# Kernel tuning notes

Measured on AMD Instinct MI355X. Metric: run time of the kernel, lower is better.

The kernel has to match this reference:

```python
import jax, jax.numpy as jnp
import numpy as np

B, N, M, DQ, DK, DV, H = 8, 1024, 1024, 512, 512, 512, 8
DS = DV // H  # dim_split = 64
NEG = -1e38


def _ln(x, g, b, eps=1e-5):
    mu = jnp.mean(x, -1, keepdims=True)
    var = jnp.mean((x - mu) ** 2, -1, keepdims=True)
    return (x - mu) * jax.lax.rsqrt(var + eps) * g + b


def setup_inputs() -> dict:
    key = jax.random.key(0)
    ks = jax.random.split(key, 16)
    s = 0.02
    return {
        "x": jax.random.normal(ks[0], (B, N, DQ), jnp.float32),
        "y": jax.random.normal(ks[1], (B, M, DK), jnp.float32),
        "x_mask": jax.random.randint(ks[2], (B, N), 0, 2).astype(bool),
        "y_mask": jax.random.randint(ks[3], (B, M), 0, 2).astype(bool),
        "Wq": jax.random.normal(ks[4], (DQ, DV), jnp.float32) * s,
        "Wk": jax.random.normal(ks[5], (DK, DV), jnp.float32) * s,
        "Wv": jax.random.normal(ks[6], (DK, DV), jnp.float32) * s,
        "Wo": jax.random.normal(ks[7], (DV, DQ), jnp.float32) * s,
        "W1": jax.random.normal(ks[8], (DQ, DQ), jnp.float32) * s,
        "b1": jnp.zeros((DQ,), jnp.float32),
        "W2": jax.random.normal(ks[9], (DQ, DQ), jnp.float32) * s,
        "b2": jnp.zeros((DQ,), jnp.float32),
        "g1": jnp.ones((DQ,), jnp.float32),
        "be1": jnp.zeros((DQ,), jnp.float32),
        "g2": jnp.ones((DQ,), jnp.float32),
        "be2": jnp.zeros((DQ,), jnp.float32),
    }


def reference(x, y, x_mask, y_mask, Wq, Wk, Wv, Wo, W1, b1, W2, b2, g1, be1, g2, be2):
    xm = x_mask[..., None]  # [B,N,1]
    ym = y_mask[..., None]  # [B,M,1]
    x = jnp.where(xm, 0.0, x)
    y = jnp.where(ym, 0.0, y)
    # projections (no bias); masked rows stay zero, re-mask as in source
    q = jnp.where(xm, 0.0, x @ Wq).reshape(B, N, H, DS)
    k = jnp.where(ym, 0.0, y @ Wk).reshape(B, M, H, DS)
    v = jnp.where(ym, 0.0, y @ Wv).reshape(B, M, H, DS)
    # scaled dot product; NOTE: scale is sqrt(dim_v), faithful to source
    sdp = jnp.einsum('bnhd,bmhd->bhnm', q, k) / np.sqrt(DV)
    mask = x_mask[:, None, :, None] | y_mask[:, None, None, :]  # [B,1,N,M]
    sdp = jnp.where(mask, NEG, sdp)
    alpha = jax.nn.softmax(sdp, axis=-1)  # softmax over keys (slot_att=False)
    att = jnp.einsum('bhnm,bmhd->bnhd', alpha, v).reshape(B, N, DV)
    att = jnp.where(xm, 0.0, att)
    o = x + att @ Wo
    o = _ln(o, g1, be1)
    ff = jax.nn.relu(o @ W1 + b1) @ W2 + b2
    o = _ln(o + ff, g2, be2)
    return jnp.where(xm, 0.0, o)
```

## Files before the change

kernel.cpp:

```cpp
#include <hip/hip_runtime.h>
#include <hip/hip_bf16.h>

typedef __bf16 bf16;
typedef __attribute__((ext_vector_type(4))) __bf16 bf16x4;
typedef __attribute__((ext_vector_type(8))) __bf16 bf16x8;
typedef __attribute__((ext_vector_type(4))) float f32x4;

#define B_ 8
#define N_ 1024
#define M_ 1024
#define H_ 8
#define ROWS_ (B_ * N_)

__device__ __forceinline__ f32x4 mfma16(bf16x8 a, bf16x8 b, f32x4 c) {
    return __builtin_amdgcn_mfma_f32_16x16x32_bf16(a, b, c, 0, 0, 0);
}

__device__ __forceinline__ void glds16(const void* g, void* l) {
    __builtin_amdgcn_global_load_lds((const __attribute__((address_space(1))) void*)g,
                                     (__attribute__((address_space(3))) void*)l, 16, 0, 0);
}

__global__ __launch_bounds__(256) void prep(const float* __restrict__ x, const float* __restrict__ y,
                                            bf16* __restrict__ Xb, bf16* __restrict__ Yb,
                                            const float* W0, const float* W1, const float* W2,
                                            const float* W3, const float* W4, const float* W5,
                                            bf16* T0, bf16* T1, bf16* T2, bf16* T3, bf16* T4, bf16* T5) {
    __shared__ float t[64][65];
    int bid = blockIdx.x;
    if (bid < 8192) {
        int i = bid * 256 + threadIdx.x;
        const float4* s;
        bf16x4* d;
        int j;
        if (i < 1048576) { s = (const float4*)x; d = (bf16x4*)Xb; j = i; }
        else             { s = (const float4*)y; d = (bf16x4*)Yb; j = i - 1048576; }
        float4 f = s[j];
        bf16x4 o = {(bf16)f.x, (bf16)f.y, (bf16)f.z, (bf16)f.w};
        d[j] = o;
        return;
    }
    int wb = bid - 8192;
    const float* srcs[6] = {W0, W1, W2, W3, W4, W5};
    bf16* dsts[6] = {T0, T1, T2, T3, T4, T5};
    const float* W = srcs[wb >> 6];
    bf16* Wt = dsts[wb >> 6];
    int tile = wb & 63;
    int k0 = (tile >> 3) * 64, n0 = (tile & 7) * 64;
    int tx = threadIdx.x & 63, ty = threadIdx.x >> 6;
#pragma unroll
    for (int j = 0; j < 16; ++j)
        t[ty + j * 4][tx] = W[(size_t)(k0 + ty + j * 4) * 512 + n0 + tx];
    __syncthreads();
#pragma unroll
    for (int j = 0; j < 16; ++j)
        Wt[(size_t)(n0 + ty + j * 4) * 512 + k0 + tx] = (bf16)t[tx][ty + j * 4];
}

__device__ __forceinline__ void gemm_core(const bf16* __restrict__ A, const bf16* __restrict__ Bt,
                                          int row0, int col0, bf16* As, bf16* Bs, f32x4 acc[2][4]) {
    int tid = threadIdx.x, wave = tid >> 6, lane = tid & 63;
    int lr = lane & 15, q4 = lane >> 4;
    const bf16* Asrc[4];
    const bf16* Bsrc[2];
#pragma unroll
    for (int s = 0; s < 4; ++s) {
        int c = tid + s * 256, r = c >> 3, bk = (c & 7) ^ (r & 7);
        Asrc[s] = A + (size_t)(row0 + r) * 512 + bk * 8;
    }
#pragma unroll
    for (int s = 0; s < 2; ++s) {
        int c = tid + s * 256, r = c >> 3, bk = (c & 7) ^ (r & 7);
        Bsrc[s] = Bt + (size_t)(col0 + r) * 512 + bk * 8;
    }
    int wb = wave * 1024;
    for (int k0 = 0; k0 < 512; k0 += 64) {
        __syncthreads();
#pragma unroll
        for (int s = 0; s < 4; ++s) glds16(Asrc[s] + k0, (char*)As + s * 4096 + wb);
#pragma unroll
        for (int s = 0; s < 2; ++s) glds16(Bsrc[s] + k0, (char*)Bs + s * 4096 + wb);
        __syncthreads();
        bf16x8 af[2][2], bfr[4][2];
#pragma unroll
        for (int rt = 0; rt < 2; ++rt) {
            int row = wave * 32 + rt * 16 + lr;
#pragma unroll
            for (int c = 0; c < 2; ++c)
                af[rt][c] = *(const bf16x8*)((const char*)As + (row * 8 + ((c * 4 + q4) ^ (row & 7))) * 16);
        }
#pragma unroll
        for (int ct = 0; ct < 4; ++ct) {
            int col = ct * 16 + lr;
#pragma unroll
            for (int c = 0; c < 2; ++c)
                bfr[ct][c] = *(const bf16x8*)((const char*)Bs + (col * 8 + ((c * 4 + q4) ^ (col & 7))) * 16);
        }
#pragma unroll
        for (int rt = 0; rt < 2; ++rt)
#pragma unroll
            for (int ct = 0; ct < 4; ++ct) {
                acc[rt][ct] = mfma16(af[rt][0], bfr[ct][0], acc[rt][ct]);
                acc[rt][ct] = mfma16(af[rt][1], bfr[ct][1], acc[rt][ct]);
            }
    }
}

__global__ __launch_bounds__(256) void proj_qkv(const bf16* __restrict__ Xb, const bf16* __restrict__ Yb,
                                                const bf16* __restrict__ Wqt, const bf16* __restrict__ Wkt,
                                                const bf16* __restrict__ Wvt,
                                                bf16* __restrict__ qb, bf16* __restrict__ kb,
                                                bf16* __restrict__ Vt) {
    __shared__ bf16 As[128 * 64];
    __shared__ bf16 Bs[64 * 64];
    int z = blockIdx.z;
    const bf16 *A, *Bt;
    int row0, col0;
    if (z == 0)      { A = Xb;  Bt = Wqt; row0 = blockIdx.x * 128; col0 = blockIdx.y * 64; }
    else if (z == 1) { A = Yb;  Bt = Wkt; row0 = blockIdx.x * 128; col0 = blockIdx.y * 64; }
    else { A = Wvt; Bt = Yb; int flat = blockIdx.y * 64 + blockIdx.x; row0 = (flat & 3) * 128; col0 = (flat >> 2) * 64; }
    const f32x4 z4 = {0.f, 0.f, 0.f, 0.f};
    f32x4 acc[2][4] = {{z4, z4, z4, z4}, {z4, z4, z4, z4}};
    gemm_core(A, Bt, row0, col0, As, Bs, acc);
    int wave = threadIdx.x >> 6, lane = threadIdx.x & 63, lr = lane & 15, q4 = lane >> 4;
    bf16* dst = (z == 0) ? qb : kb;
#pragma unroll
    for (int rt = 0; rt < 2; ++rt)
#pragma unroll
        for (int ct = 0; ct < 4; ++ct) {
            int col = col0 + ct * 16 + lr;
#pragma unroll
            for (int r = 0; r < 4; ++r) {
                int row = row0 + wave * 32 + rt * 16 + q4 * 4 + r;
                bf16 v = (bf16)acc[rt][ct][r];
                if (z < 2) dst[(size_t)row * 512 + col] = v;
                else Vt[(size_t)((col >> 10) * 512 + row) * 1024 + (col & 1023)] = v;
            }
        }
}

template <int MODE>
__global__ __launch_bounds__(256) void gemm_bt(const bf16* __restrict__ A, const bf16* __restrict__ Bt,
                                               const float* __restrict__ bias, void* __restrict__ Cout) {
    __shared__ bf16 As[128 * 64];
    __shared__ bf16 Bs[64 * 64];
    int row0 = blockIdx.x * 128, col0 = blockIdx.y * 64;
    const f32x4 z4 = {0.f, 0.f, 0.f, 0.f};
    f32x4 acc[2][4] = {{z4, z4, z4, z4}, {z4, z4, z4, z4}};
    gemm_core(A, Bt, row0, col0, As, Bs, acc);
    int wave = threadIdx.x >> 6, lane = threadIdx.x & 63, lr = lane & 15, q4 = lane >> 4;
#pragma unroll
    for (int rt = 0; rt < 2; ++rt)
#pragma unroll
        for (int ct = 0; ct < 4; ++ct) {
            int col = col0 + ct * 16 + lr;
            float bv = (MODE >= 2) ? bias[col] : 0.0f;
#pragma unroll
            for (int r = 0; r < 4; ++r) {
                int row = row0 + wave * 32 + rt * 16 + q4 * 4 + r;
                float v = acc[rt][ct][r] + bv;
                if (MODE == 3) v = fmaxf(v, 0.0f);
                if (MODE == 3) ((bf16*)Cout)[(size_t)row * 512 + col] = (bf16)v;
                else           ((float*)Cout)[(size_t)row * 512 + col] = v;
            }
        }
}

__global__ __launch_bounds__(512) void attn(const bf16* __restrict__ Q, const bf16* __restrict__ Kb,
                                            const bf16* __restrict__ Vt, const int* __restrict__ ymask,
                                            bf16* __restrict__ att) {
    __shared__ bf16 Ks[2][64 * 64];
    __shared__ bf16 Vs[2][64 * 64];
    __shared__ bf16 Ps[8][16 * 72];

    int bid = blockIdx.x;
    int bh = bid & 63, n0 = (bid >> 6) * 128;
    int b = bh >> 3, h = bh & 7;
    int tid = threadIdx.x, wave = tid >> 6, lane = tid & 63;
    int lr = lane & 15, q4 = lane >> 4;
    const float scale = 0.044194173824159216f;

    const bf16* qp = Q + (size_t)((b << 10) + n0 + wave * 16 + lr) * 512 + h * 64 + q4 * 8;
    bf16x8 aq0 = *(const bf16x8*)qp;
    bf16x8 aq1 = *(const bf16x8*)(qp + 32);

    int r = tid >> 3, bk = (tid & 7) ^ (r & 7);
    const bf16* Ksrc = Kb + (size_t)((b << 10) + r) * 512 + h * 64 + bk * 8;
    const bf16* Vsrc = Vt + (size_t)(b * 512 + h * 64 + r) * 1024 + bk * 8;
    int wb = wave * 1024;

    const f32x4 zv = {0.f, 0.f, 0.f, 0.f};
    f32x4 O[4] = {zv, zv, zv, zv};
    float lsum[4] = {0.f, 0.f, 0.f, 0.f};

    for (int m0 = 0; m0 < M_; m0 += 128) {
        int mk0 = ymask[(b << 10) + m0 + lane];
        int mk1 = ymask[(b << 10) + m0 + 64 + lane];
        __syncthreads();
        glds16(Ksrc + (size_t)m0 * 512, (char*)Ks[0] + wb);
        glds16(Ksrc + (size_t)(m0 + 64) * 512, (char*)Ks[1] + wb);
        glds16(Vsrc + m0, (char*)Vs[0] + wb);
        glds16(Vsrc + m0 + 64, (char*)Vs[1] + wb);
        __syncthreads();

#pragma unroll
        for (int half = 0; half < 2; ++half) {
            const char* K_ = (const char*)Ks[half];
            const char* V_ = (const char*)Vs[half];
            int mkh = half ? mk1 : mk0;
#pragma unroll
            for (int nt = 0; nt < 4; ++nt) {
                int krow = nt * 16 + lr;
                bf16x8 kf0 = *(const bf16x8*)(K_ + (krow * 8 + (q4 ^ (krow & 7))) * 16);
                bf16x8 kf1 = *(const bf16x8*)(K_ + (krow * 8 + ((4 + q4) ^ (krow & 7))) * 16);
                int mkv = __shfl(mkh, krow);
                f32x4 s = mfma16(aq0, kf0, zv);
                s = mfma16(aq1, kf1, s);
#pragma unroll
                for (int rr = 0; rr < 4; ++rr) {
                    float p = mkv ? 0.0f : __expf(s[rr] * scale);
                    lsum[rr] += p;
                    Ps[wave][(q4 * 4 + rr) * 72 + krow] = (bf16)p;
                }
            }
            bf16x8 ap0 = *(const bf16x8*)&Ps[wave][lr * 72 + q4 * 8];
            bf16x8 ap1 = *(const bf16x8*)&Ps[wave][lr * 72 + 32 + q4 * 8];
#pragma unroll
            for (int dt = 0; dt < 4; ++dt) {
                int vrow = dt * 16 + lr;
                bf16x8 vf0 = *(const bf16x8*)(V_ + (vrow * 8 + (q4 ^ (vrow & 7))) * 16);
                bf16x8 vf1 = *(const bf16x8*)(V_ + (vrow * 8 + ((4 + q4) ^ (vrow & 7))) * 16);
                O[dt] = mfma16(ap0, vf0, O[dt]);
                O[dt] = mfma16(ap1, vf1, O[dt]);
            }
        }
    }

#pragma unroll
    for (int rr = 0; rr < 4; ++rr) {
        float v = lsum[rr];
        v += __shfl_xor(v, 1); v += __shfl_xor(v, 2);
        v += __shfl_xor(v, 4); v += __shfl_xor(v, 8);
        lsum[rr] = (v > 0.0f) ? (1.0f / v) : 0.0f;
    }
#pragma unroll
    for (int dt = 0; dt < 4; ++dt)
#pragma unroll
        for (int rr = 0; rr < 4; ++rr) {
            int row = n0 + wave * 16 + q4 * 4 + rr;
            att[(size_t)((b << 10) + row) * 512 + h * 64 + dt * 16 + lr] =
                (bf16)(O[dt][rr] * lsum[rr]);
        }
}

__global__ __launch_bounds__(256) void ln1_k(const float* __restrict__ X, const float* __restrict__ R,
                                             const float* __restrict__ g, const float* __restrict__ be,
                                             float* __restrict__ O, bf16* __restrict__ Obf) {
    int row = blockIdx.x, t = threadIdx.x;
    size_t base = (size_t)row * 512;
    float t0 = X[base + t] + R[base + t];
    float t1 = X[base + 256 + t] + R[base + 256 + t];
    float s = t0 + t1, sq = t0 * t0 + t1 * t1;
#pragma unroll
    for (int off = 1; off < 64; off <<= 1) { s += __shfl_xor(s, off); sq += __shfl_xor(sq, off); }
    __shared__ float ls[4], lq[4];
    int w = t >> 6;
    if ((t & 63) == 0) { ls[w] = s; lq[w] = sq; }
    __syncthreads();
    s = ls[0] + ls[1] + ls[2] + ls[3];
    sq = lq[0] + lq[1] + lq[2] + lq[3];
    float mu = s * (1.0f / 512.0f);
    float var = sq * (1.0f / 512.0f) - mu * mu;
    float rs = rsqrtf(var + 1e-5f);
    float o0 = (t0 - mu) * rs * g[t] + be[t];
    float o1 = (t1 - mu) * rs * g[256 + t] + be[256 + t];
    O[base + t] = o0; O[base + 256 + t] = o1;
    Obf[base + t] = (bf16)o0; Obf[base + 256 + t] = (bf16)o1;
}

__global__ __launch_bounds__(256) void ln2_k(const float* __restrict__ O, const float* __restrict__ F,
                                             const float* __restrict__ g, const float* __restrict__ be,
                                             const int* __restrict__ xmask, float* __restrict__ out) {
    int row = blockIdx.x, t = threadIdx.x;
    size_t base = (size_t)row * 512;
    float t0 = O[base + t] + F[base + t];
    float t1 = O[base + 256 + t] + F[base + 256 + t];
    float s = t0 + t1, sq = t0 * t0 + t1 * t1;
#pragma unroll
    for (int off = 1; off < 64; off <<= 1) { s += __shfl_xor(s, off); sq += __shfl_xor(sq, off); }
    __shared__ float ls[4], lq[4];
    int w = t >> 6;
    if ((t & 63) == 0) { ls[w] = s; lq[w] = sq; }
    __syncthreads();
    s = ls[0] + ls[1] + ls[2] + ls[3];
    sq = lq[0] + lq[1] + lq[2] + lq[3];
    float mu = s * (1.0f / 512.0f);
    float var = sq * (1.0f / 512.0f) - mu * mu;
    float rs = rsqrtf(var + 1e-5f);
    int msk = xmask[row];
    float o0 = (t0 - mu) * rs * g[t] + be[t];
    float o1 = (t1 - mu) * rs * g[256 + t] + be[256 + t];
    out[base + t] = msk ? 0.0f : o0;
    out[base + 256 + t] = msk ? 0.0f : o1;
}

extern "C" void kernel_launch(void* const* d_in, const int* in_sizes, int n_in,
                              void* d_out, int out_size, void* d_ws, size_t ws_size,
                              hipStream_t stream) {
    const float* x   = (const float*)d_in[0];
    const float* y   = (const float*)d_in[1];
    const int*   xm  = (const int*)d_in[2];
    const int*   ym  = (const int*)d_in[3];
    const float* Wq  = (const float*)d_in[4];
    const float* Wk  = (const float*)d_in[5];
    const float* Wv  = (const float*)d_in[6];
    const float* Wo  = (const float*)d_in[7];
    const float* W1  = (const float*)d_in[8];
    const float* b1  = (const float*)d_in[9];
    const float* W2  = (const float*)d_in[10];
    const float* b2  = (const float*)d_in[11];
    const float* g1  = (const float*)d_in[12];
    const float* be1 = (const float*)d_in[13];
    const float* g2  = (const float*)d_in[14];
    const float* be2 = (const float*)d_in[15];

    char* ws = (char*)d_ws;
    const size_t WT_SZ  = 512 * 512 * sizeof(bf16);
    const size_t XB_SZ  = (size_t)ROWS_ * 512 * sizeof(bf16);
    const size_t F32_SZ = (size_t)ROWS_ * 512 * sizeof(float);

    bf16* Wqt = (bf16*)(ws + 0 * WT_SZ);
    bf16* Wkt = (bf16*)(ws + 1 * WT_SZ);
    bf16* Wvt = (bf16*)(ws + 2 * WT_SZ);
    bf16* Wot = (bf16*)(ws + 3 * WT_SZ);
    bf16* W1t = (bf16*)(ws + 4 * WT_SZ);
    bf16* W2t = (bf16*)(ws + 5 * WT_SZ);
    size_t off = 6 * WT_SZ;
    bf16* Xb  = (bf16*)(ws + off); off += XB_SZ;
    bf16* Yb  = (bf16*)(ws + off); off += XB_SZ;
    bf16* qb  = (bf16*)(ws + off); off += XB_SZ;
    bf16* kb  = (bf16*)(ws + off); off += XB_SZ;
    bf16* Vt  = (bf16*)(ws + off); off += XB_SZ;
    float* awo = (float*)(ws + off); off += F32_SZ;
    float* ob  = (float*)(ws + off); off += F32_SZ;
    bf16* attb = Xb;
    bf16* obf  = qb;
    bf16* hb   = Yb;
    float* fb  = awo;

    prep<<<8576, 256, 0, stream>>>(x, y, Xb, Yb, Wq, Wk, Wv, Wo, W1, W2,
                                   Wqt, Wkt, Wvt, Wot, W1t, W2t);

    proj_qkv<<<dim3(64, 8, 3), 256, 0, stream>>>(Xb, Yb, Wqt, Wkt, Wvt, qb, kb, Vt);

    attn<<<512, 512, 0, stream>>>(qb, kb, Vt, ym, attb);

    dim3 gg(64, 8);
    gemm_bt<0><<<gg, 256, 0, stream>>>(attb, Wot, nullptr, awo);
    ln1_k<<<ROWS_, 256, 0, stream>>>(x, awo, g1, be1, ob, obf);
    gemm_bt<3><<<gg, 256, 0, stream>>>(obf, W1t, b1, hb);
    gemm_bt<2><<<gg, 256, 0, stream>>>(hb, W2t, b2, fb);
    ln2_k<<<ROWS_, 256, 0, stream>>>(ob, fb, g2, be2, xm, (float*)d_out);
}
```

Baseline: 218.2 us.

## Enlarge GEMM and attention register tiles, vectorize layernorm kernels

```diff
diff --git a/kernel.cpp b/kernel.cpp
--- a/kernel.cpp
+++ b/kernel.cpp
@@ -58,46 +58,42 @@
 }
 
 __device__ __forceinline__ void gemm_core(const bf16* __restrict__ A, const bf16* __restrict__ Bt,
-                                          int row0, int col0, bf16* As, bf16* Bs, f32x4 acc[2][4]) {
+                                          int row0, int col0, bf16* As, bf16* Bs, f32x4 acc[4][4]) {
     int tid = threadIdx.x, wave = tid >> 6, lane = tid & 63;
     int lr = lane & 15, q4 = lane >> 4;
-    const bf16* Asrc[4];
-    const bf16* Bsrc[2];
+    const bf16 *Asrc[4], *Bsrc[4];
 #pragma unroll
     for (int s = 0; s < 4; ++s) {
         int c = tid + s * 256, r = c >> 3, bk = (c & 7) ^ (r & 7);
         Asrc[s] = A + (size_t)(row0 + r) * 512 + bk * 8;
-    }
-#pragma unroll
-    for (int s = 0; s < 2; ++s) {
-        int c = tid + s * 256, r = c >> 3, bk = (c & 7) ^ (r & 7);
         Bsrc[s] = Bt + (size_t)(col0 + r) * 512 + bk * 8;
     }
     int wb = wave * 1024;
+    int rbase = (wave & 1) * 64, cbase = (wave >> 1) * 64;
     for (int k0 = 0; k0 < 512; k0 += 64) {
         __syncthreads();
 #pragma unroll
         for (int s = 0; s < 4; ++s) glds16(Asrc[s] + k0, (char*)As + s * 4096 + wb);
 #pragma unroll
-        for (int s = 0; s < 2; ++s) glds16(Bsrc[s] + k0, (char*)Bs + s * 4096 + wb);
+        for (int s = 0; s < 4; ++s) glds16(Bsrc[s] + k0, (char*)Bs + s * 4096 + wb);
         __syncthreads();
-        bf16x8 af[2][2], bfr[4][2];
-#pragma unroll
-        for (int rt = 0; rt < 2; ++rt) {
-            int row = wave * 32 + rt * 16 + lr;
+        bf16x8 af[4][2], bfr[4][2];
+#pragma unroll
+        for (int rt = 0; rt < 4; ++rt) {
+            int row = rbase + rt * 16 + lr;
 #pragma unroll
             for (int c = 0; c < 2; ++c)
                 af[rt][c] = *(const bf16x8*)((const char*)As + (row * 8 + ((c * 4 + q4) ^ (row & 7))) * 16);
         }
 #pragma unroll
         for (int ct = 0; ct < 4; ++ct) {
-            int col = ct * 16 + lr;
+            int col = cbase + ct * 16 + lr;
 #pragma unroll
             for (int c = 0; c < 2; ++c)
                 bfr[ct][c] = *(const bf16x8*)((const char*)Bs + (col * 8 + ((c * 4 + q4) ^ (col & 7))) * 16);
         }
 #pragma unroll
-        for (int rt = 0; rt < 2; ++rt)
+        for (int rt = 0; rt < 4; ++rt)
 #pragma unroll
             for (int ct = 0; ct < 4; ++ct) {
                 acc[rt][ct] = mfma16(af[rt][0], bfr[ct][0], acc[rt][ct]);
@@ -106,32 +102,37 @@
     }
 }
 
-__global__ __launch_bounds__(256) void proj_qkv(const bf16* __restrict__ Xb, const bf16* __restrict__ Yb,
-                                                const bf16* __restrict__ Wqt, const bf16* __restrict__ Wkt,
-                                                const bf16* __restrict__ Wvt,
-                                                bf16* __restrict__ qb, bf16* __restrict__ kb,
-                                                bf16* __restrict__ Vt) {
+__global__ __launch_bounds__(256, 2) void proj_qkv(const bf16* __restrict__ Xb, const bf16* __restrict__ Yb,
+                                                   const bf16* __restrict__ Wqt, const bf16* __restrict__ Wkt,
+                                                   const bf16* __restrict__ Wvt,
+                                                   bf16* __restrict__ qb, bf16* __restrict__ kb,
+                                                   bf16* __restrict__ Vt) {
     __shared__ bf16 As[128 * 64];
-    __shared__ bf16 Bs[64 * 64];
+    __shared__ bf16 Bs[128 * 64];
     int z = blockIdx.z;
     const bf16 *A, *Bt;
     int row0, col0;
-    if (z == 0)      { A = Xb;  Bt = Wqt; row0 = blockIdx.x * 128; col0 = blockIdx.y * 64; }
-    else if (z == 1) { A = Yb;  Bt = Wkt; row0 = blockIdx.x * 128; col0 = blockIdx.y * 64; }
-    else { A = Wvt; Bt = Yb; int flat = blockIdx.y * 64 + blockIdx.x; row0 = (flat & 3) * 128; col0 = (flat >> 2) * 64; }
+    if (z == 0)      { A = Xb;  Bt = Wqt; row0 = blockIdx.x * 128; col0 = blockIdx.y * 128; }
+    else if (z == 1) { A = Yb;  Bt = Wkt; row0 = blockIdx.x * 128; col0 = blockIdx.y * 128; }
+    else { A = Wvt; Bt = Yb; int flat = blockIdx.y * 64 + blockIdx.x; row0 = (flat & 3) * 128; col0 = (flat >> 2) * 128; }
     const f32x4 z4 = {0.f, 0.f, 0.f, 0.f};
-    f32x4 acc[2][4] = {{z4, z4, z4, z4}, {z4, z4, z4, z4}};
+    f32x4 acc[4][4];
+#pragma unroll
+    for (int rt = 0; rt < 4; ++rt)
+#pragma unroll
+        for (int ct = 0; ct < 4; ++ct) acc[rt][ct] = z4;
     gemm_core(A, Bt, row0, col0, As, Bs, acc);
     int wave = threadIdx.x >> 6, lane = threadIdx.x & 63, lr = lane & 15, q4 = lane >> 4;
+    int rbase = (wave & 1) * 64, cbase = (wave >> 1) * 64;
     bf16* dst = (z == 0) ? qb : kb;
 #pragma unroll
-    for (int rt = 0; rt < 2; ++rt)
+    for (int rt = 0; rt < 4; ++rt)
 #pragma unroll
         for (int ct = 0; ct < 4; ++ct) {
-            int col = col0 + ct * 16 + lr;
+            int col = col0 + cbase + ct * 16 + lr;
 #pragma unroll
             for (int r = 0; r < 4; ++r) {
-                int row = row0 + wave * 32 + rt * 16 + q4 * 4 + r;
+                int row = row0 + rbase + rt * 16 + q4 * 4 + r;
                 bf16 v = (bf16)acc[rt][ct][r];
                 if (z < 2) dst[(size_t)row * 512 + col] = v;
                 else Vt[(size_t)((col >> 10) * 512 + row) * 1024 + (col & 1023)] = v;
@@ -140,24 +141,29 @@
 }
 
 template <int MODE>
-__global__ __launch_bounds__(256) void gemm_bt(const bf16* __restrict__ A, const bf16* __restrict__ Bt,
-                                               const float* __restrict__ bias, void* __restrict__ Cout) {
+__global__ __launch_bounds__(256, 2) void gemm_bt(const bf16* __restrict__ A, const bf16* __restrict__ Bt,
+                                                  const float* __restrict__ bias, void* __restrict__ Cout) {
     __shared__ bf16 As[128 * 64];
-    __shared__ bf16 Bs[64 * 64];
-    int row0 = blockIdx.x * 128, col0 = blockIdx.y * 64;
+    __shared__ bf16 Bs[128 * 64];
+    int row0 = blockIdx.x * 128, col0 = blockIdx.y * 128;
     const f32x4 z4 = {0.f, 0.f, 0.f, 0.f};
-    f32x4 acc[2][4] = {{z4, z4, z4, z4}, {z4, z4, z4, z4}};
+    f32x4 acc[4][4];
+#pragma unroll
+    for (int rt = 0; rt < 4; ++rt)
+#pragma unroll
+        for (int ct = 0; ct < 4; ++ct) acc[rt][ct] = z4;
     gemm_core(A, Bt, row0, col0, As, Bs, acc);
     int wave = threadIdx.x >> 6, lane = threadIdx.x & 63, lr = lane & 15, q4 = lane >> 4;
-#pragma unroll
-    for (int rt = 0; rt < 2; ++rt)
+    int rbase = (wave & 1) * 64, cbase = (wave >> 1) * 64;
+#pragma unroll
+    for (int rt = 0; rt < 4; ++rt)
 #pragma unroll
         for (int ct = 0; ct < 4; ++ct) {
-            int col = col0 + ct * 16 + lr;
+            int col = col0 + cbase + ct * 16 + lr;
             float bv = (MODE >= 2) ? bias[col] : 0.0f;
 #pragma unroll
             for (int r = 0; r < 4; ++r) {
-                int row = row0 + wave * 32 + rt * 16 + q4 * 4 + r;
+                int row = row0 + rbase + rt * 16 + q4 * 4 + r;
                 float v = acc[rt][ct][r] + bv;
                 if (MODE == 3) v = fmaxf(v, 0.0f);
                 if (MODE == 3) ((bf16*)Cout)[(size_t)row * 512 + col] = (bf16)v;
@@ -166,12 +172,12 @@
         }
 }
 
-__global__ __launch_bounds__(512) void attn(const bf16* __restrict__ Q, const bf16* __restrict__ Kb,
-                                            const bf16* __restrict__ Vt, const int* __restrict__ ymask,
-                                            bf16* __restrict__ att) {
-    __shared__ bf16 Ks[2][64 * 64];
-    __shared__ bf16 Vs[2][64 * 64];
-    __shared__ bf16 Ps[8][16 * 72];
+__global__ __launch_bounds__(256, 2) void attn(const bf16* __restrict__ Q, const bf16* __restrict__ Kb,
+                                               const bf16* __restrict__ Vt, const int* __restrict__ ymask,
+                                               bf16* __restrict__ att) {
+    __shared__ bf16 Ks[64 * 64];
+    __shared__ bf16 Vs[64 * 64];
+    __shared__ bf16 Ps[4][32 * 72];
 
     int bid = blockIdx.x;
     int bh = bid & 63, n0 = (bid >> 6) * 128;
@@ -180,128 +186,154 @@
     int lr = lane & 15, q4 = lane >> 4;
     const float scale = 0.044194173824159216f;
 
-    const bf16* qp = Q + (size_t)((b << 10) + n0 + wave * 16 + lr) * 512 + h * 64 + q4 * 8;
-    bf16x8 aq0 = *(const bf16x8*)qp;
-    bf16x8 aq1 = *(const bf16x8*)(qp + 32);
-
-    int r = tid >> 3, bk = (tid & 7) ^ (r & 7);
-    const bf16* Ksrc = Kb + (size_t)((b << 10) + r) * 512 + h * 64 + bk * 8;
-    const bf16* Vsrc = Vt + (size_t)(b * 512 + h * 64 + r) * 1024 + bk * 8;
+    bf16x8 aq[2][2];
+#pragma unroll
+    for (int rt = 0; rt < 2; ++rt) {
+        const bf16* qp = Q + (size_t)((b << 10) + n0 + wave * 32 + rt * 16 + lr) * 512 + h * 64 + q4 * 8;
+        aq[rt][0] = *(const bf16x8*)qp;
+        aq[rt][1] = *(const bf16x8*)(qp + 32);
+    }
+
+    const bf16 *Ksrc[2], *Vsrc[2];
+#pragma unroll
+    for (int s = 0; s < 2; ++s) {
+        int c = tid + s * 256, r = c >> 3, bk = (c & 7) ^ (r & 7);
+        Ksrc[s] = Kb + (size_t)((b << 10) + r) * 512 + h * 64 + bk * 8;
+        Vsrc[s] = Vt + (size_t)(b * 512 + h * 64 + r) * 1024 + bk * 8;
+    }
     int wb = wave * 1024;
 
     const f32x4 zv = {0.f, 0.f, 0.f, 0.f};
-    f32x4 O[4] = {zv, zv, zv, zv};
-    float lsum[4] = {0.f, 0.f, 0.f, 0.f};
-
-    for (int m0 = 0; m0 < M_; m0 += 128) {
-        int mk0 = ymask[(b << 10) + m0 + lane];
-        int mk1 = ymask[(b << 10) + m0 + 64 + lane];
+    f32x4 O[2][4];
+    float lsum[2][4];
+#pragma unroll
+    for (int rt = 0; rt < 2; ++rt) {
+#pragma unroll
+        for (int dt = 0; dt < 4; ++dt) O[rt][dt] = zv;
+#pragma unroll
+        for (int rr = 0; rr < 4; ++rr) lsum[rt][rr] = 0.f;
+    }
+
+    for (int m0 = 0; m0 < M_; m0 += 64) {
+        int mk = ymask[(b << 10) + m0 + lane];
         __syncthreads();
-        glds16(Ksrc + (size_t)m0 * 512, (char*)Ks[0] + wb);
-        glds16(Ksrc + (size_t)(m0 + 64) * 512, (char*)Ks[1] + wb);
-        glds16(Vsrc + m0, (char*)Vs[0] + wb);
-        glds16(Vsrc + m0 + 64, (char*)Vs[1] + wb);
+#pragma unroll
+        for (int s = 0; s < 2; ++s) {
+            glds16(Ksrc[s] + (size_t)m0 * 512, (char*)Ks + s * 4096 + wb);
+            glds16(Vsrc[s] + m0, (char*)Vs + s * 4096 + wb);
+        }
         __syncthreads();
 
 #pragma unroll
-        for (int half = 0; half < 2; ++half) {
-            const char* K_ = (const char*)Ks[half];
-            const char* V_ = (const char*)Vs[half];
-            int mkh = half ? mk1 : mk0;
-#pragma unroll
-            for (int nt = 0; nt < 4; ++nt) {
-                int krow = nt * 16 + lr;
-                bf16x8 kf0 = *(const bf16x8*)(K_ + (krow * 8 + (q4 ^ (krow & 7))) * 16);
-                bf16x8 kf1 = *(const bf16x8*)(K_ + (krow * 8 + ((4 + q4) ^ (krow & 7))) * 16);
-                int mkv = __shfl(mkh, krow);
-                f32x4 s = mfma16(aq0, kf0, zv);
-                s = mfma16(aq1, kf1, s);
+        for (int nt = 0; nt < 4; ++nt) {
+            int krow = nt * 16 + lr;
+            bf16x8 kf0 = *(const bf16x8*)((const char*)Ks + (krow * 8 + (q4 ^ (krow & 7))) * 16);
+            bf16x8 kf1 = *(const bf16x8*)((const char*)Ks + (krow * 8 + ((4 + q4) ^ (krow & 7))) * 16);
+            int mkv = __shfl(mk, krow);
+#pragma unroll
+            for (int rt = 0; rt < 2; ++rt) {
+                f32x4 s = mfma16(aq[rt][0], kf0, zv);
+                s = mfma16(aq[rt][1], kf1, s);
 #pragma unroll
                 for (int rr = 0; rr < 4; ++rr) {
                     float p = mkv ? 0.0f : __expf(s[rr] * scale);
-                    lsum[rr] += p;
-                    Ps[wave][(q4 * 4 + rr) * 72 + krow] = (bf16)p;
+                    lsum[rt][rr] += p;
+                    Ps[wave][(rt * 16 + q4 * 4 + rr) * 72 + krow] = (bf16)p;
                 }
             }
-            bf16x8 ap0 = *(const bf16x8*)&Ps[wave][lr * 72 + q4 * 8];
-            bf16x8 ap1 = *(const bf16x8*)&Ps[wave][lr * 72 + 32 + q4 * 8];
-#pragma unroll
-            for (int dt = 0; dt < 4; ++dt) {
-                int vrow = dt * 16 + lr;
-                bf16x8 vf0 = *(const bf16x8*)(V_ + (vrow * 8 + (q4 ^ (vrow & 7))) * 16);
-                bf16x8 vf1 = *(const bf16x8*)(V_ + (vrow * 8 + ((4 + q4) ^ (vrow & 7))) * 16);
-                O[dt] = mfma16(ap0, vf0, O[dt]);
-                O[dt] = mfma16(ap1, vf1, O[dt]);
-            }
-        }
-    }
-
-#pragma unroll
-    for (int rr = 0; rr < 4; ++rr) {
-        float v = lsum[rr];
-        v += __shfl_xor(v, 1); v += __shfl_xor(v, 2);
-        v += __shfl_xor(v, 4); v += __shfl_xor(v, 8);
-        lsum[rr] = (v > 0.0f) ? (1.0f / v) : 0.0f;
-    }
-#pragma unroll
-    for (int dt = 0; dt < 4; ++dt)
+        }
+        bf16x8 ap[2][2];
+#pragma unroll
+        for (int rt = 0; rt < 2; ++rt) {
+            ap[rt][0] = *(const bf16x8*)&Ps[wave][(rt * 16 + lr) * 72 + q4 * 8];
+            ap[rt][1] = *(const bf16x8*)&Ps[wave][(rt * 16 + lr) * 72 + 32 + q4 * 8];
+        }
+#pragma unroll
+        for (int dt = 0; dt < 4; ++dt) {
+            int vrow = dt * 16 + lr;
+            bf16x8 vf0 = *(const bf16x8*)((const char*)Vs + (vrow * 8 + (q4 ^ (vrow & 7))) * 16);
+            bf16x8 vf1 = *(const bf16x8*)((const char*)Vs + (vrow * 8 + ((4 + q4) ^ (vrow & 7))) * 16);
+#pragma unroll
+            for (int rt = 0; rt < 2; ++rt) {
+                O[rt][dt] = mfma16(ap[rt][0], vf0, O[rt][dt]);
+                O[rt][dt] = mfma16(ap[rt][1], vf1, O[rt][dt]);
+            }
+        }
+    }
+
+#pragma unroll
+    for (int rt = 0; rt < 2; ++rt)
 #pragma unroll
         for (int rr = 0; rr < 4; ++rr) {
-            int row = n0 + wave * 16 + q4 * 4 + rr;
-            att[(size_t)((b << 10) + row) * 512 + h * 64 + dt * 16 + lr] =
-                (bf16)(O[dt][rr] * lsum[rr]);
-        }
-}
-
-__global__ __launch_bounds__(256) void ln1_k(const float* __restrict__ X, const float* __restrict__ R,
+            float v = lsum[rt][rr];
+            v += __shfl_xor(v, 1); v += __shfl_xor(v, 2);
+            v += __shfl_xor(v, 4); v += __shfl_xor(v, 8);
+            lsum[rt][rr] = (v > 0.0f) ? (1.0f / v) : 0.0f;
+        }
+#pragma unroll
+    for (int rt = 0; rt < 2; ++rt)
+#pragma unroll
+        for (int dt = 0; dt < 4; ++dt)
+#pragma unroll
+            for (int rr = 0; rr < 4; ++rr) {
+                int row = n0 + wave * 32 + rt * 16 + q4 * 4 + rr;
+                att[(size_t)((b << 10) + row) * 512 + h * 64 + dt * 16 + lr] =
+                    (bf16)(O[rt][dt][rr] * lsum[rt][rr]);
+            }
+}
+
+__global__ __launch_bounds__(128) void ln1_k(const float* __restrict__ X, const float* __restrict__ R,
                                              const float* __restrict__ g, const float* __restrict__ be,
                                              float* __restrict__ O, bf16* __restrict__ Obf) {
     int row = blockIdx.x, t = threadIdx.x;
-    size_t base = (size_t)row * 512;
-    float t0 = X[base + t] + R[base + t];
-    float t1 = X[base + 256 + t] + R[base + 256 + t];
-    float s = t0 + t1, sq = t0 * t0 + t1 * t1;
+    float4 xv = ((const float4*)(X + (size_t)row * 512))[t];
+    float4 rv = ((const float4*)(R + (size_t)row * 512))[t];
+    float4 o = {xv.x + rv.x, xv.y + rv.y, xv.z + rv.z, xv.w + rv.w};
+    float s = o.x + o.y + o.z + o.w;
+    float sq = o.x * o.x + o.y * o.y + o.z * o.z + o.w * o.w;
 #pragma unroll
     for (int off = 1; off < 64; off <<= 1) { s += __shfl_xor(s, off); sq += __shfl_xor(sq, off); }
-    __shared__ float ls[4], lq[4];
-    int w = t >> 6;
-    if ((t & 63) == 0) { ls[w] = s; lq[w] = sq; }
+    __shared__ float ls[2], lq[2];
+    if ((t & 63) == 0) { ls[t >> 6] = s; lq[t >> 6] = sq; }
     __syncthreads();
-    s = ls[0] + ls[1] + ls[2] + ls[3];
-    sq = lq[0] + lq[1] + lq[2] + lq[3];
+    s = ls[0] + ls[1]; sq = lq[0] + lq[1];
     float mu = s * (1.0f / 512.0f);
     float var = sq * (1.0f / 512.0f) - mu * mu;
     float rs = rsqrtf(var + 1e-5f);
-    float o0 = (t0 - mu) * rs * g[t] + be[t];
-    float o1 = (t1 - mu) * rs * g[256 + t] + be[256 + t];
-    O[base + t] = o0; O[base + 256 + t] = o1;
-    Obf[base + t] = (bf16)o0; Obf[base + 256 + t] = (bf16)o1;
-}
-
-__global__ __launch_bounds__(256) void ln2_k(const float* __restrict__ O, const float* __restrict__ F,
+    float4 gv = ((const float4*)g)[t];
+    float4 bv = ((const float4*)be)[t];
+    float4 r4 = {(o.x - mu) * rs * gv.x + bv.x, (o.y - mu) * rs * gv.y + bv.y,
+                 (o.z - mu) * rs * gv.z + bv.z, (o.w - mu) * rs * gv.w + bv.w};
+    ((float4*)(O + (size_t)row * 512))[t] = r4;
+    bf16x4 b4 = {(bf16)r4.x, (bf16)r4.y, (bf16)r4.z, (bf16)r4.w};
+    ((bf16x4*)(Obf + (size_t)row * 512))[t] = b4;
+}
+
+__global__ __launch_bounds__(128) void ln2_k(const float* __restrict__ O, const float* __restrict__ F,
                                              const float* __restrict__ g, const float* __restrict__ be,
                                              const int* __restrict__ xmask, float* __restrict__ out) {
     int row = blockIdx.x, t = threadIdx.x;
-    size_t base = (size_t)row * 512;
-    float t0 = O[base + t] + F[base + t];
-    float t1 = O[base + 256 + t] + F[base + 256 + t];
-    float s = t0 + t1, sq = t0 * t0 + t1 * t1;
+    float4 xv = ((const float4*)(O + (size_t)row * 512))[t];
+    float4 rv = ((const float4*)(F + (size_t)row * 512))[t];
+    float4 o = {xv.x + rv.x, xv.y + rv.y, xv.z + rv.z, xv.w + rv.w};
+    float s = o.x + o.y + o.z + o.w;
+    float sq = o.x * o.x + o.y * o.y + o.z * o.z + o.w * o.w;
 #pragma unroll
     for (int off = 1; off < 64; off <<= 1) { s += __shfl_xor(s, off); sq += __shfl_xor(sq, off); }
-    __shared__ float ls[4], lq[4];
-    int w = t >> 6;
-    if ((t & 63) == 0) { ls[w] = s; lq[w] = sq; }
+    __shared__ float ls[2], lq[2];
+    if ((t & 63) == 0) { ls[t >> 6] = s; lq[t >> 6] = sq; }
     __syncthreads();
-    s = ls[0] + ls[1] + ls[2] + ls[3];
-    sq = lq[0] + lq[1] + lq[2] + lq[3];
+    s = ls[0] + ls[1]; sq = lq[0] + lq[1];
     float mu = s * (1.0f / 512.0f);
     float var = sq * (1.0f / 512.0f) - mu * mu;
     float rs = rsqrtf(var + 1e-5f);
     int msk = xmask[row];
-    float o0 = (t0 - mu) * rs * g[t] + be[t];
-    float o1 = (t1 - mu) * rs * g[256 + t] + be[256 + t];
-    out[base + t] = msk ? 0.0f : o0;
-    out[base + 256 + t] = msk ? 0.0f : o1;
+    float4 gv = ((const float4*)g)[t];
+    float4 bv = ((const float4*)be)[t];
+    float4 r4 = {(o.x - mu) * rs * gv.x + bv.x, (o.y - mu) * rs * gv.y + bv.y,
+                 (o.z - mu) * rs * gv.z + bv.z, (o.w - mu) * rs * gv.w + bv.w};
+    if (msk) r4 = {0.f, 0.f, 0.f, 0.f};
+    ((float4*)(out + (size_t)row * 512))[t] = r4;
 }
 
 extern "C" void kernel_launch(void* const* d_in, const int* in_sizes, int n_in,
@@ -351,14 +383,14 @@
     prep<<<8576, 256, 0, stream>>>(x, y, Xb, Yb, Wq, Wk, Wv, Wo, W1, W2,
                                    Wqt, Wkt, Wvt, Wot, W1t, W2t);
 
-    proj_qkv<<<dim3(64, 8, 3), 256, 0, stream>>>(Xb, Yb, Wqt, Wkt, Wvt, qb, kb, Vt);
-
-    attn<<<512, 512, 0, stream>>>(qb, kb, Vt, ym, attb);
-
-    dim3 gg(64, 8);
+    proj_qkv<<<dim3(64, 4, 3), 256, 0, stream>>>(Xb, Yb, Wqt, Wkt, Wvt, qb, kb, Vt);
+
+    attn<<<512, 256, 0, stream>>>(qb, kb, Vt, ym, attb);
+
+    dim3 gg(64, 4);
     gemm_bt<0><<<gg, 256, 0, stream>>>(attb, Wot, nullptr, awo);
-    ln1_k<<<ROWS_, 256, 0, stream>>>(x, awo, g1, be1, ob, obf);
+    ln1_k<<<ROWS_, 128, 0, stream>>>(x, awo, g1, be1, ob, obf);
     gemm_bt<3><<<gg, 256, 0, stream>>>(obf, W1t, b1, hb);
     gemm_bt<2><<<gg, 256, 0, stream>>>(hb, W2t, b2, fb);
-    ln2_k<<<ROWS_, 256, 0, stream>>>(ob, fb, g2, be2, xm, (float*)d_out);
-}
+    ln2_k<<<ROWS_, 128, 0, stream>>>(ob, fb, g2, be2, xm, (float*)d_out);
+}
```

After: 221.3 us. No clear change (+1.4%).
